# Kernel tuning notes

Measured on AMD Instinct MI355X. Metric: run time of the kernel, lower is better.

The kernel has to match this reference:

```python
import jax, jax.numpy as jnp
import numpy as np

B, L, D = 1, 4096, 1024
H = 16
HD = D // H
SCALE = HD ** -0.5


def setup_inputs() -> dict:
    key = jax.random.key(0)
    k1, k2, k3 = jax.random.split(key, 3)
    X = jax.random.normal(k1, (B, L, D), dtype=jnp.float32)
    # torch Linear default init ~ U(-1/sqrt(fan_in), 1/sqrt(fan_in)); scaled normals are fine for a reference
    Wqkv = jax.random.normal(k2, (D, 3 * D), dtype=jnp.float32) * (D ** -0.5)
    bqkv = jnp.zeros((3 * D,), dtype=jnp.float32)
    Wproj = jax.random.normal(k3, (D, D), dtype=jnp.float32) * (D ** -0.5)
    bproj = jnp.zeros((D,), dtype=jnp.float32)
    return {"X": X, "Wqkv": Wqkv, "bqkv": bqkv, "Wproj": Wproj, "bproj": bproj}


def reference(X, Wqkv, bqkv, Wproj, bproj):
    Bn, Ln, Dn = X.shape
    qkv = X @ Wqkv + bqkv                       # [B, L, 3D]
    qkv = qkv.reshape(Bn, Ln, 3, H, HD)
    q, k, v = qkv[:, :, 0], qkv[:, :, 1], qkv[:, :, 2]   # [B, L, H, HD]
    # attention scores [B, H, L, L] (naive, matches original)
    attn = jnp.einsum('bqhd,bkhd->bhqk', q, k) * SCALE
    causal = jnp.tril(jnp.ones((Ln, Ln), dtype=bool))     # True = keep
    attn = jnp.where(causal, attn, -jnp.inf)
    score = jax.nn.softmax(attn, axis=-1)
    out = jnp.einsum('bhqk,bkhd->bqhd', score, v)         # [B, L, H, HD]
    out = out.reshape(Bn, Ln, Dn)
    return out @ Wproj + bproj
```

## Files before the change

kernel.cpp:

```cpp
#include <hip/hip_runtime.h>
#include <hip/hip_bf16.h>
#include <string.h>


typedef unsigned short ushort_t;
typedef __attribute__((ext_vector_type(8))) short short8;
typedef __attribute__((ext_vector_type(4))) float f32x4;

#define MFMA16(a, b, c) __builtin_amdgcn_mfma_f32_16x16x32_bf16(a, b, c, 0, 0, 0)

static constexpr int Lq = 4096;
static constexpr int Dm = 1024;
static constexpr int NH = 16;
static constexpr int HD = 64;
static constexpr int D3 = 3072;
static constexpr float SCALE_LOG2E = 0.125f * 1.44269504088896340736f;

__device__ __forceinline__ ushort_t f2bf(float f) {
    union { float f; unsigned int u; } x{f};
    unsigned int u = x.u;
    u += 0x7fffu + ((u >> 16) & 1u);
    return (ushort_t)(u >> 16);
}

__device__ __forceinline__ unsigned int cvtpk(float a, float b) {
    __hip_bfloat162 h = __float22bfloat162_rn(make_float2(a, b));
    unsigned int u;
    memcpy(&u, &h, 4);
    return u;
}

__device__ __forceinline__ void gl2lds16(const ushort_t* g, ushort_t* l) {
    __builtin_amdgcn_global_load_lds(
        (const __attribute__((address_space(1))) unsigned int*)g,
        (__attribute__((address_space(3))) unsigned int*)l, 16, 0, 0);
}

__global__ void cvt_bf16(const float* __restrict__ in, ushort_t* __restrict__ out, int n) {
    int i = (blockIdx.x * blockDim.x + threadIdx.x) * 4;
    if (i + 3 < n) {
        float4 v = *(const float4*)&in[i];
        ushort_t r[4] = { f2bf(v.x), f2bf(v.y), f2bf(v.z), f2bf(v.w) };
        *(uint2*)&out[i] = *(uint2*)r;
    }
}

__global__ void wtrans(const float* __restrict__ W, ushort_t* __restrict__ Wt, int K, int N) {
    __shared__ float tile[32][33];
    int nb = blockIdx.x * 32, kb = blockIdx.y * 32;
    int tx = threadIdx.x, ty = threadIdx.y;
    for (int j = 0; j < 32; j += 8)
        tile[ty + j][tx] = W[(size_t)(kb + ty + j) * N + nb + tx];
    __syncthreads();
    for (int j = 0; j < 32; j += 8)
        Wt[(size_t)(nb + ty + j) * K + kb + tx] = f2bf(tile[tx][ty + j]);
}

__global__ void vtrans(const ushort_t* __restrict__ qkv, ushort_t* __restrict__ Vt) {
    __shared__ ushort_t tile[32][33];
    int h  = blockIdx.z;
    int lb = blockIdx.x * 32;
    int db = blockIdx.y * 32;
    int tx = threadIdx.x, ty = threadIdx.y;
    for (int j = 0; j < 32; j += 8)
        tile[ty + j][tx] = qkv[(size_t)(lb + ty + j) * D3 + 2048 + h * HD + db + tx];
    __syncthreads();
    const int key  = lb + tx;
    const int k63  = key & 63;
    const int cp   = (key & ~63) + ((k63 & 15) * 4 + (k63 >> 4));
    for (int j = 0; j < 32; j += 8)
        Vt[(size_t)h * HD * Lq + (size_t)(db + ty + j) * Lq + cp] = tile[tx][ty + j];
}

template <bool OUT_BF16, bool QSCALE>
__global__ void __launch_bounds__(256)
gemm_bt(const ushort_t* __restrict__ A, const ushort_t* __restrict__ Bt,
        const float* __restrict__ bias, void* __restrict__ C,
        int M, int N, int K) {
    __shared__ alignas(16) ushort_t Alds[128 * 32];
    __shared__ alignas(16) ushort_t Blds[128 * 32];
    const int tid  = threadIdx.x;
    const int lane = tid & 63;
    const int w    = tid >> 6;
    const int quad = lane >> 4;
    const int l16  = lane & 15;
    const int mbase = blockIdx.x * 128;
    const int nbase = blockIdx.y * 128;
    const int moff  = (w >> 1) * 64;
    const int noff  = (w & 1) * 64;

    f32x4 acc[4][4] = {};

    for (int kb = 0; kb < K; kb += 32) {
        __syncthreads();
        #pragma unroll
        for (int c = 0; c < 2; c++) {
            int id  = w * 128 + c * 64 + lane;
            int row = id >> 2, col = (id & 3) * 8;
            gl2lds16(&A[(size_t)(mbase + row) * K + kb + col], &Alds[(size_t)(w * 128 + c * 64) * 8]);
            gl2lds16(&Bt[(size_t)(nbase + row) * K + kb + col], &Blds[(size_t)(w * 128 + c * 64) * 8]);
        }
        __syncthreads();
        short8 a[4], b[4];
        #pragma unroll
        for (int m = 0; m < 4; m++)
            a[m] = *(const short8*)&Alds[(moff + m * 16 + l16) * 32 + quad * 8];
        #pragma unroll
        for (int n = 0; n < 4; n++)
            b[n] = *(const short8*)&Blds[(noff + n * 16 + l16) * 32 + quad * 8];
        #pragma unroll
        for (int m = 0; m < 4; m++)
            #pragma unroll
            for (int n = 0; n < 4; n++)
                acc[m][n] = MFMA16(a[m], b[n], acc[m][n]);
    }

    #pragma unroll
    for (int m = 0; m < 4; m++)
        #pragma unroll
        for (int n = 0; n < 4; n++)
            #pragma unroll
            for (int r = 0; r < 4; r++) {
                int row = mbase + moff + m * 16 + quad * 4 + r;
                int col = nbase + noff + n * 16 + l16;
                float v = acc[m][n][r] + bias[col];
                if (QSCALE && col < Dm) v *= SCALE_LOG2E;
                if (OUT_BF16)
                    ((ushort_t*)C)[(size_t)row * N + col] = f2bf(v);
                else
                    ((float*)C)[(size_t)row * N + col] = v;
            }
}

__global__ void __launch_bounds__(256, 2)
attn_fwd(const ushort_t* __restrict__ qkv, const ushort_t* __restrict__ Vt,
         ushort_t* __restrict__ O) {
    __shared__ alignas(16) ushort_t Kl[2][64 * 64];
    __shared__ alignas(16) ushort_t Vl[2][64 * 64];
    __shared__ alignas(16) ushort_t Pl[4 * 32 * 72];

    const int tid  = threadIdx.x;
    const int lane = tid & 63;
    const int w    = tid >> 6;
    const int quad = lane >> 4;
    const int l16  = lane & 15;
    const int bid  = blockIdx.x;
    const int h    = bid & 15;
    const int c    = 31 - (bid >> 4);
    const int qc   = c * 128;
    const int qw   = qc + w * 32;
    ushort_t* pw   = Pl + w * 32 * 72;
    const float NEG_INF = -__builtin_inff();
    const int sw   = l16 & 7;

    const short bf1 = (short)0x3F80;
    const short8 ones = { bf1, bf1, bf1, bf1, bf1, bf1, bf1, bf1 };

    const ushort_t* kbase = qkv + Dm + h * HD;
    const ushort_t* vbase = Vt + (size_t)h * HD * Lq;

    short8 qf[2][2];
    #pragma unroll
    for (int m = 0; m < 2; m++) {
        const ushort_t* qr = qkv + (size_t)(qw + m * 16 + l16) * D3 + h * HD;
        qf[m][0] = *(const short8*)(qr + quad * 8);
        qf[m][1] = *(const short8*)(qr + 32 + quad * 8);
    }

    f32x4 o[2][4] = {};
    f32x4 lacc[2] = {};

    int kvo[4][2];
    #pragma unroll
    for (int s = 0; s < 4; s++)
        #pragma unroll
        for (int kh = 0; kh < 2; kh++)
            kvo[s][kh] = (s * 16 + l16) * 64 + (((kh * 4 + quad) ^ sw) * 8);

    const int g0 = w * 128 + lane;
    const int r0 = g0 >> 3, c0 = (g0 & 7) ^ (r0 & 7);
    const int g1 = g0 + 64;
    const int r1 = g1 >> 3, c1 = (g1 & 7) ^ (r1 & 7);
    const ushort_t* ks0 = kbase + (size_t)r0 * D3 + c0 * 8;
    const ushort_t* ks1 = kbase + (size_t)r1 * D3 + c1 * 8;
    const ushort_t* vs0 = vbase + (size_t)r0 * Lq + c0 * 8;
    const ushort_t* vs1 = vbase + (size_t)r1 * Lq + c1 * 8;

    auto stage = [&](int t, int b) {
        const size_t ko = (size_t)t * 64 * D3;
        const int    vo = t * 64;
        gl2lds16(ks0 + ko, &Kl[b][w * 1024]);
        gl2lds16(ks1 + ko, &Kl[b][w * 1024 + 512]);
        gl2lds16(vs0 + vo, &Vl[b][w * 1024]);
        gl2lds16(vs1 + vo, &Vl[b][w * 1024 + 512]);
    };

    auto compute = [&](const ushort_t* Kb, const ushort_t* Vb, int k0, bool domask) {
        short8 kf[4][2];
        #pragma unroll
        for (int s = 0; s < 4; s++)
            #pragma unroll
            for (int kh = 0; kh < 2; kh++)
                kf[s][kh] = *(const short8*)&Kb[kvo[s][kh]];

        f32x4 st[2][4];
        #pragma unroll
        for (int m = 0; m < 2; m++)
            #pragma unroll
            for (int s = 0; s < 4; s++) {
                f32x4 t = {};
                t = MFMA16(qf[m][0], kf[s][0], t);
                t = MFMA16(qf[m][1], kf[s][1], t);
                st[m][s] = t;
            }

        #pragma unroll
        for (int m = 0; m < 2; m++)
            #pragma unroll
            for (int r = 0; r < 4; r++) {
                float e[4];
                #pragma unroll
                for (int s = 0; s < 4; s++) {
                    float v = st[m][s][r];
                    if (domask) {
                        const int qg = qw + m * 16 + quad * 4 + r;
                        if (k0 + s * 16 + l16 > qg) v = NEG_INF;
                    }
                    e[s] = __builtin_amdgcn_exp2f(v);
                }
                uint2 pk = { cvtpk(e[0], e[1]), cvtpk(e[2], e[3]) };
                *(uint2*)&pw[(m * 16 + quad * 4 + r) * 72 + l16 * 4] = pk;
            }

        short8 pf[2][2];
        #pragma unroll
        for (int m = 0; m < 2; m++)
            #pragma unroll
            for (int kh = 0; kh < 2; kh++)
                pf[m][kh] = *(const short8*)&pw[(m * 16 + l16) * 72 + kh * 32 + quad * 8];
        #pragma unroll
        for (int m = 0; m < 2; m++) {
            lacc[m] = MFMA16(pf[m][0], ones, lacc[m]);
            lacc[m] = MFMA16(pf[m][1], ones, lacc[m]);
        }

        short8 vf[4][2];
        #pragma unroll
        for (int t = 0; t < 4; t++)
            #pragma unroll
            for (int kh = 0; kh < 2; kh++)
                vf[t][kh] = *(const short8*)&Vb[kvo[t][kh]];
        #pragma unroll
        for (int m = 0; m < 2; m++)
            #pragma unroll
            for (int t = 0; t < 4; t++) {
                o[m][t] = MFMA16(pf[m][0], vf[t][0], o[m][t]);
                o[m][t] = MFMA16(pf[m][1], vf[t][1], o[m][t]);
            }
    };

    stage(0, 0);

    for (int kt2 = 0; kt2 < c; kt2++) {
        __syncthreads();
        stage(2 * kt2 + 1, 1);
        compute(Kl[0], Vl[0], (2 * kt2) * 64, false);
        __syncthreads();
        stage(2 * kt2 + 2, 0);
        compute(Kl[1], Vl[1], (2 * kt2 + 1) * 64, false);
    }
    __syncthreads();
    stage(2 * c + 1, 1);
    compute(Kl[0], Vl[0], 2 * c * 64, true);
    __syncthreads();
    compute(Kl[1], Vl[1], 2 * c * 64 + 64, true);

    #pragma unroll
    for (int m = 0; m < 2; m++)
        #pragma unroll
        for (int r = 0; r < 4; r++) {
            const float inv = 1.0f / lacc[m][r];
            ushort_t* orow = O + (size_t)(qw + m * 16 + quad * 4 + r) * Dm + h * HD;
            #pragma unroll
            for (int t = 0; t < 4; t++)
                orow[t * 16 + l16] = f2bf(o[m][t][r] * inv);
        }
}

extern "C" void kernel_launch(void* const* d_in, const int* in_sizes, int n_in,
                              void* d_out, int out_size, void* d_ws, size_t ws_size,
                              hipStream_t stream) {
    const float* X     = (const float*)d_in[0];
    const float* Wqkv  = (const float*)d_in[1];
    const float* bqkv  = (const float*)d_in[2];
    const float* Wproj = (const float*)d_in[3];
    const float* bproj = (const float*)d_in[4];
    float* out = (float*)d_out;

    ushort_t* ws     = (ushort_t*)d_ws;
    ushort_t* Xb     = ws;
    ushort_t* WqkvT  = Xb + (size_t)Lq * Dm;
    ushort_t* WprojT = WqkvT + (size_t)D3 * Dm;
    ushort_t* qkvB   = WprojT + (size_t)Dm * Dm;
    ushort_t* VtB    = qkvB + (size_t)Lq * D3;
    ushort_t* Ob     = VtB + (size_t)NH * HD * Lq;

    cvt_bf16<<<(Lq * Dm / 4 + 255) / 256, 256, 0, stream>>>(X, Xb, Lq * Dm);
    wtrans<<<dim3(D3 / 32, Dm / 32), dim3(32, 8), 0, stream>>>(Wqkv, WqkvT, Dm, D3);
    wtrans<<<dim3(Dm / 32, Dm / 32), dim3(32, 8), 0, stream>>>(Wproj, WprojT, Dm, Dm);

    gemm_bt<true, true><<<dim3(Lq / 128, D3 / 128), 256, 0, stream>>>(
        Xb, WqkvT, bqkv, (void*)qkvB, Lq, D3, Dm);

    vtrans<<<dim3(Lq / 32, HD / 32, NH), dim3(32, 8), 0, stream>>>(qkvB, VtB);

    attn_fwd<<<dim3(512), 256, 0, stream>>>(qkvB, VtB, Ob);

    gemm_bt<false, false><<<dim3(Lq / 128, Dm / 128), 256, 0, stream>>>(
        Ob, WprojT, bproj, (void*)out, Lq, Dm, Dm);
}
```

Before: 232.7 us.

## Pair causal query chunks per block and split KV range across two wave groups

The attention kernel now launches 256 blocks of 512 threads. Each block handles two query chunks (p and 31-p), so every block gets the same total amount of causal work. Within a block, two groups of four waves each process alternating 64-key tiles, and their partial O and row-sum accumulators are combined through shared memory before normalisation. This targets the load imbalance of causal tiles and doubles the parallelism per query chunk, at the cost of more LDS, extra reduction syncs and fewer blocks.

```diff
diff --git a/kernel.cpp b/kernel.cpp
--- a/kernel.cpp
+++ b/kernel.cpp
@@ -132,23 +132,24 @@
             }
 }
 
-__global__ void __launch_bounds__(256, 2)
+__global__ void __launch_bounds__(512, 2)
 attn_fwd(const ushort_t* __restrict__ qkv, const ushort_t* __restrict__ Vt,
          ushort_t* __restrict__ O) {
-    __shared__ alignas(16) ushort_t Kl[2][64 * 64];
-    __shared__ alignas(16) ushort_t Vl[2][64 * 64];
-    __shared__ alignas(16) ushort_t Pl[4 * 32 * 72];
+    __shared__ alignas(16) ushort_t Kl[2][2][64 * 64];
+    __shared__ alignas(16) ushort_t Vl[2][2][64 * 64];
+    __shared__ alignas(16) ushort_t Pl[8 * 32 * 72];
+    __shared__ alignas(16) float    Ml[256 * 41];
 
     const int tid  = threadIdx.x;
     const int lane = tid & 63;
     const int w    = tid >> 6;
+    const int half = w >> 2;
+    const int sub  = w & 3;
     const int quad = lane >> 4;
     const int l16  = lane & 15;
     const int bid  = blockIdx.x;
     const int h    = bid & 15;
-    const int c    = 31 - (bid >> 4);
-    const int qc   = c * 128;
-    const int qw   = qc + w * 32;
+    const int p    = bid >> 4;
     ushort_t* pw   = Pl + w * 32 * 72;
     const float NEG_INF = -__builtin_inff();
     const int sw   = l16 & 7;
@@ -159,17 +160,6 @@
     const ushort_t* kbase = qkv + Dm + h * HD;
     const ushort_t* vbase = Vt + (size_t)h * HD * Lq;
 
-    short8 qf[2][2];
-    #pragma unroll
-    for (int m = 0; m < 2; m++) {
-        const ushort_t* qr = qkv + (size_t)(qw + m * 16 + l16) * D3 + h * HD;
-        qf[m][0] = *(const short8*)(qr + quad * 8);
-        qf[m][1] = *(const short8*)(qr + 32 + quad * 8);
-    }
-
-    f32x4 o[2][4] = {};
-    f32x4 lacc[2] = {};
-
     int kvo[4][2];
     #pragma unroll
     for (int s = 0; s < 4; s++)
@@ -177,114 +167,149 @@
         for (int kh = 0; kh < 2; kh++)
             kvo[s][kh] = (s * 16 + l16) * 64 + (((kh * 4 + quad) ^ sw) * 8);
 
-    const int g0 = w * 128 + lane;
-    const int r0 = g0 >> 3, c0 = (g0 & 7) ^ (r0 & 7);
-    const int g1 = g0 + 64;
-    const int r1 = g1 >> 3, c1 = (g1 & 7) ^ (r1 & 7);
-    const ushort_t* ks0 = kbase + (size_t)r0 * D3 + c0 * 8;
-    const ushort_t* ks1 = kbase + (size_t)r1 * D3 + c1 * 8;
-    const ushort_t* vs0 = vbase + (size_t)r0 * Lq + c0 * 8;
-    const ushort_t* vs1 = vbase + (size_t)r1 * Lq + c1 * 8;
-
-    auto stage = [&](int t, int b) {
-        const size_t ko = (size_t)t * 64 * D3;
-        const int    vo = t * 64;
-        gl2lds16(ks0 + ko, &Kl[b][w * 1024]);
-        gl2lds16(ks1 + ko, &Kl[b][w * 1024 + 512]);
-        gl2lds16(vs0 + vo, &Vl[b][w * 1024]);
-        gl2lds16(vs1 + vo, &Vl[b][w * 1024 + 512]);
-    };
-
-    auto compute = [&](const ushort_t* Kb, const ushort_t* Vb, int k0, bool domask) {
-        short8 kf[4][2];
-        #pragma unroll
-        for (int s = 0; s < 4; s++)
-            #pragma unroll
-            for (int kh = 0; kh < 2; kh++)
-                kf[s][kh] = *(const short8*)&Kb[kvo[s][kh]];
-
-        f32x4 st[2][4];
-        #pragma unroll
-        for (int m = 0; m < 2; m++)
-            #pragma unroll
-            for (int s = 0; s < 4; s++) {
-                f32x4 t = {};
-                t = MFMA16(qf[m][0], kf[s][0], t);
-                t = MFMA16(qf[m][1], kf[s][1], t);
-                st[m][s] = t;
+    const int rr = tid >> 3, cc = (tid & 7) ^ (rr & 7);
+    const ushort_t* kse = kbase + (size_t)rr * D3 + cc * 8;
+    const ushort_t* vse = vbase + (size_t)rr * Lq + cc * 8;
+    const int dstoff = w * 512;
+
+    for (int sel = 0; sel < 2; sel++) {
+        const int c      = sel ? (31 - p) : p;
+        const int qc     = c * 128;
+        const int rounds = c + 1;
+        const int qw     = qc + sub * 32;
+
+        short8 qf[2][2];
+        #pragma unroll
+        for (int m = 0; m < 2; m++) {
+            const ushort_t* qr = qkv + (size_t)(qw + m * 16 + l16) * D3 + h * HD;
+            qf[m][0] = *(const short8*)(qr + quad * 8);
+            qf[m][1] = *(const short8*)(qr + 32 + quad * 8);
+        }
+
+        f32x4 o[2][4] = {};
+        f32x4 lacc[2] = {};
+
+        const ushort_t* kp = kse;
+        const ushort_t* vp = vse;
+
+        auto stage = [&](int b) {
+            gl2lds16(kp,            &Kl[0][b][dstoff]);
+            gl2lds16(kp + 64 * D3,  &Kl[1][b][dstoff]);
+            gl2lds16(vp,            &Vl[0][b][dstoff]);
+            gl2lds16(vp + 64,       &Vl[1][b][dstoff]);
+            kp += (size_t)128 * D3;
+            vp += 128;
+        };
+
+        stage(0);
+
+        for (int r = 0; r < rounds; r++) {
+            const int buf = r & 1;
+            __syncthreads();
+            if (r + 1 < rounds) stage(buf ^ 1);
+
+            const ushort_t* Kb = &Kl[half][buf][0];
+            const ushort_t* Vb = &Vl[half][buf][0];
+            const int k0 = (2 * r + half) * 64;
+            const bool domask = (r == rounds - 1);
+
+            short8 kf[4][2];
+            #pragma unroll
+            for (int s = 0; s < 4; s++)
+                #pragma unroll
+                for (int kh = 0; kh < 2; kh++)
+                    kf[s][kh] = *(const short8*)&Kb[kvo[s][kh]];
+
+            f32x4 st[2][4];
+            #pragma unroll
+            for (int m = 0; m < 2; m++)
+                #pragma unroll
+                for (int s = 0; s < 4; s++) {
+                    f32x4 t = {};
+                    t = MFMA16(qf[m][0], kf[s][0], t);
+                    t = MFMA16(qf[m][1], kf[s][1], t);
+                    st[m][s] = t;
+                }
+
+            #pragma unroll
+            for (int m = 0; m < 2; m++)
+                #pragma unroll
+                for (int r4 = 0; r4 < 4; r4++) {
+                    float e[4];
+                    #pragma unroll
+                    for (int s = 0; s < 4; s++) {
+                        float v = st[m][s][r4];
+                        if (domask) {
+                            const int qg = qw + m * 16 + quad * 4 + r4;
+                            if (k0 + s * 16 + l16 > qg) v = NEG_INF;
+                        }
+                        e[s] = __builtin_amdgcn_exp2f(v);
+                    }
+                    uint2 pk = { cvtpk(e[0], e[1]), cvtpk(e[2], e[3]) };
+                    *(uint2*)&pw[(m * 16 + quad * 4 + r4) * 72 + l16 * 4] = pk;
+                }
+
+            short8 pf[2][2];
+            #pragma unroll
+            for (int m = 0; m < 2; m++)
+                #pragma unroll
+                for (int kh = 0; kh < 2; kh++)
+                    pf[m][kh] = *(const short8*)&pw[(m * 16 + l16) * 72 + kh * 32 + quad * 8];
+            #pragma unroll
+            for (int m = 0; m < 2; m++) {
+                lacc[m] = MFMA16(pf[m][0], ones, lacc[m]);
+                lacc[m] = MFMA16(pf[m][1], ones, lacc[m]);
             }
 
-        #pragma unroll
-        for (int m = 0; m < 2; m++)
-            #pragma unroll
-            for (int r = 0; r < 4; r++) {
-                float e[4];
-                #pragma unroll
-                for (int s = 0; s < 4; s++) {
-                    float v = st[m][s][r];
-                    if (domask) {
-                        const int qg = qw + m * 16 + quad * 4 + r;
-                        if (k0 + s * 16 + l16 > qg) v = NEG_INF;
-                    }
-                    e[s] = __builtin_amdgcn_exp2f(v);
+            short8 vf[4][2];
+            #pragma unroll
+            for (int t = 0; t < 4; t++)
+                #pragma unroll
+                for (int kh = 0; kh < 2; kh++)
+                    vf[t][kh] = *(const short8*)&Vb[kvo[t][kh]];
+            #pragma unroll
+            for (int m = 0; m < 2; m++)
+                #pragma unroll
+                for (int t = 0; t < 4; t++) {
+                    o[m][t] = MFMA16(pf[m][0], vf[t][0], o[m][t]);
+                    o[m][t] = MFMA16(pf[m][1], vf[t][1], o[m][t]);
                 }
-                uint2 pk = { cvtpk(e[0], e[1]), cvtpk(e[2], e[3]) };
-                *(uint2*)&pw[(m * 16 + quad * 4 + r) * 72 + l16 * 4] = pk;
-            }
-
-        short8 pf[2][2];
-        #pragma unroll
-        for (int m = 0; m < 2; m++)
-            #pragma unroll
-            for (int kh = 0; kh < 2; kh++)
-                pf[m][kh] = *(const short8*)&pw[(m * 16 + l16) * 72 + kh * 32 + quad * 8];
-        #pragma unroll
-        for (int m = 0; m < 2; m++) {
-            lacc[m] = MFMA16(pf[m][0], ones, lacc[m]);
-            lacc[m] = MFMA16(pf[m][1], ones, lacc[m]);
-        }
-
-        short8 vf[4][2];
-        #pragma unroll
-        for (int t = 0; t < 4; t++)
-            #pragma unroll
-            for (int kh = 0; kh < 2; kh++)
-                vf[t][kh] = *(const short8*)&Vb[kvo[t][kh]];
-        #pragma unroll
-        for (int m = 0; m < 2; m++)
-            #pragma unroll
-            for (int t = 0; t < 4; t++) {
-                o[m][t] = MFMA16(pf[m][0], vf[t][0], o[m][t]);
-                o[m][t] = MFMA16(pf[m][1], vf[t][1], o[m][t]);
-            }
-    };
-
-    stage(0, 0);
-
-    for (int kt2 = 0; kt2 < c; kt2++) {
-        __syncthreads();
-        stage(2 * kt2 + 1, 1);
-        compute(Kl[0], Vl[0], (2 * kt2) * 64, false);
-        __syncthreads();
-        stage(2 * kt2 + 2, 0);
-        compute(Kl[1], Vl[1], (2 * kt2 + 1) * 64, false);
+        }
+
+        __syncthreads();
+        if (half == 1) {
+            float* dst = Ml + (sub * 64 + lane) * 41;
+            #pragma unroll
+            for (int m = 0; m < 2; m++)
+                #pragma unroll
+                for (int t = 0; t < 4; t++)
+                    *(f32x4*)(dst + m * 16 + t * 4) = o[m][t];
+            *(f32x4*)(dst + 32) = lacc[0];
+            *(f32x4*)(dst + 36) = lacc[1];
+        }
+        __syncthreads();
+        if (half == 0) {
+            const float* src = Ml + (sub * 64 + lane) * 41;
+            #pragma unroll
+            for (int m = 0; m < 2; m++)
+                #pragma unroll
+                for (int t = 0; t < 4; t++)
+                    o[m][t] += *(const f32x4*)(src + m * 16 + t * 4);
+            lacc[0] += *(const f32x4*)(src + 32);
+            lacc[1] += *(const f32x4*)(src + 36);
+            #pragma unroll
+            for (int m = 0; m < 2; m++)
+                #pragma unroll
+                for (int r4 = 0; r4 < 4; r4++) {
+                    const float inv = 1.0f / lacc[m][r4];
+                    ushort_t* orow = O + (size_t)(qw + m * 16 + quad * 4 + r4) * Dm + h * HD;
+                    #pragma unroll
+                    for (int t = 0; t < 4; t++)
+                        orow[t * 16 + l16] = f2bf(o[m][t][r4] * inv);
+                }
+        }
+        __syncthreads();
     }
-    __syncthreads();
-    stage(2 * c + 1, 1);
-    compute(Kl[0], Vl[0], 2 * c * 64, true);
-    __syncthreads();
-    compute(Kl[1], Vl[1], 2 * c * 64 + 64, true);
-
-    #pragma unroll
-    for (int m = 0; m < 2; m++)
-        #pragma unroll
-        for (int r = 0; r < 4; r++) {
-            const float inv = 1.0f / lacc[m][r];
-            ushort_t* orow = O + (size_t)(qw + m * 16 + quad * 4 + r) * Dm + h * HD;
-            #pragma unroll
-            for (int t = 0; t < 4; t++)
-                orow[t * 16 + l16] = f2bf(o[m][t][r] * inv);
-        }
 }
 
 extern "C" void kernel_launch(void* const* d_in, const int* in_sizes, int n_in,
@@ -314,7 +339,7 @@
 
     vtrans<<<dim3(Lq / 32, HD / 32, NH), dim3(32, 8), 0, stream>>>(qkvB, VtB);
 
-    attn_fwd<<<dim3(512), 256, 0, stream>>>(qkvB, VtB, Ob);
+    attn_fwd<<<dim3(256), 512, 0, stream>>>(qkvB, VtB, Ob);
 
     gemm_bt<false, false><<<dim3(Lq / 128, Dm / 128), 256, 0, stream>>>(
         Ob, WprojT, bproj, (void*)out, Lq, Dm, Dm);
```

Measured after the change: 222.5 us. -4.3%, faster.
